# Performance work log

Hardware: AMD Instinct MI355X
Metric: run time of the kernel (lower is better)

The kernel has to match this reference:

```python
import jax, jax.numpy as jnp
import numpy as np

N, E, F_IN, H, C = 100000, 1600000, 128, 128, 40
BN_EPS = 1e-5


def setup_inputs() -> dict:
    key = jax.random.key(0)
    ks = jax.random.split(key, 8)
    x = jax.random.normal(ks[0], (N, F_IN), dtype=jnp.float32)
    edge_index = jax.random.randint(ks[1], (2, E), 0, N, dtype=jnp.int32)
    W1 = jax.random.normal(ks[2], (F_IN, H), dtype=jnp.float32) / np.sqrt(F_IN).astype(np.float32)
    b1 = jnp.zeros((H,), jnp.float32)
    gamma = jnp.ones((H,), jnp.float32)
    beta = jnp.zeros((H,), jnp.float32)
    W2 = jax.random.normal(ks[3], (H, C), dtype=jnp.float32) / np.sqrt(H).astype(np.float32)
    b2 = jnp.zeros((C,), jnp.float32)
    return {"x": x, "edge_index": edge_index, "W1": W1, "b1": b1,
            "gamma": gamma, "beta": beta, "W2": W2, "b2": b2}


def _gcn_conv(h, src, dst, norm, W, b, n):
    # H' = D^-1/2 (A+I) D^-1/2 H W + b   (self-loops already in src/dst/norm)
    h = h @ W                                   # [N, out] small GEMM
    msg = h[src] * norm[:, None]                # [E+N, out] gather
    return jax.ops.segment_sum(msg, dst, num_segments=n) + b


def reference(x, edge_index, W1, b1, gamma, beta, W2, b2):
    n = x.shape[0]
    loop = jnp.arange(n, dtype=edge_index.dtype)
    src = jnp.concatenate([edge_index[0], loop])
    dst = jnp.concatenate([edge_index[1], loop])
    # symmetric normalization of A_tilde = A + I
    deg = jax.ops.segment_sum(jnp.ones_like(dst, jnp.float32), dst, num_segments=n)
    dis = jnp.where(deg > 0, jax.lax.rsqrt(jnp.maximum(deg, 1.0)), 0.0)
    norm = dis[src] * dis[dst]                  # [E+N]

    h = _gcn_conv(x, src, dst, norm, W1, b1, n)
    h = jax.nn.relu(h)
    # BatchNorm1d over nodes (batch statistics; eval, dropout disabled)
    mean = jnp.mean(h, axis=0)
    var = jnp.var(h, axis=0)
    h = (h - mean) * jax.lax.rsqrt(var + BN_EPS) * gamma + beta

    h = _gcn_conv(h, src, dst, norm, W2, b2, n)
    return jax.nn.log_softmax(h, axis=1)
```

## Files before the change

### kernel.cpp

```cpp
#include <hip/hip_runtime.h>
#include <math.h>

#define N_NODES 100000
#define N_EDGES 1600000
#define F_IN 128
#define H_DIM 128
#define C_OUT 40
#define BN_EPS 1e-5f

#define ELL_W 64
#define CNT_STRIDE 16

#define BKT_W 512
#define NBKT ((N_NODES + BKT_W - 1) / BKT_W)
#define BKT_CAP 12288
#define P_EDGES 2048
#define P_NB ((N_EDGES + P_EDGES - 1) / P_EDGES)
#define FP_WCV_NB 64
#define FP_XQ_NB 6250

#define G1_ROWS 128
#define G1_LD 136
#define G1_NB ((N_NODES + G1_ROWS - 1) / G1_ROWS)
#define PS_LD 800
#define G2_ROWS 128
#define G2_NB ((N_NODES + G2_ROWS - 1) / G2_ROWS)
#define H2_B 64

typedef unsigned short u16;
typedef unsigned int u32;
typedef signed char s8;
typedef __attribute__((ext_vector_type(8))) __bf16 bf16x8;
typedef __attribute__((ext_vector_type(4))) float f32x4;

__device__ __forceinline__ u16 f2bf(float f) {
    u32 u = __float_as_uint(f);
    u += 0x7FFFu + ((u >> 16) & 1u);
    return (u16)(u >> 16);
}
__device__ __forceinline__ void qfma4(float* a, u32 d, float w) {
    a[0] = fmaf((float)((int)(d << 24) >> 24), w, a[0]);
    a[1] = fmaf((float)((int)(d << 16) >> 24), w, a[1]);
    a[2] = fmaf((float)((int)(d <<  8) >> 24), w, a[2]);
    a[3] = fmaf((float)((int)d >> 24),         w, a[3]);
}
__device__ __forceinline__ u32 pack4(int q0, int q1, int q2, int q3) {
    return (u32)(q0 & 255) | ((u32)(q1 & 255) << 8) |
           ((u32)(q2 & 255) << 16) | ((u32)(q3 & 255) << 24);
}

__global__ __launch_bounds__(256) void fused_prep(const float* __restrict__ x,
                                                  const float* __restrict__ W1,
                                                  const int* __restrict__ src,
                                                  const int* __restrict__ dst,
                                                  int* __restrict__ bcur,
                                                  int2* __restrict__ region,
                                                  s8* __restrict__ xq,
                                                  float* __restrict__ qs1,
                                                  u16* __restrict__ W1t) {
    __shared__ int lcnt[NBKT];
    __shared__ int gofs[NBKT];
    int b = blockIdx.x, t = threadIdx.x;
    if (b < P_NB) {
        for (int i = t; i < NBKT; i += 256) lcnt[i] = 0;
        __syncthreads();
        int base = b * P_EDGES;
        int d[8], bk[8];
        #pragma unroll
        for (int i = 0; i < 8; ++i) {
            int idx = base + i * 256 + t;
            if (idx < N_EDGES) {
                d[i] = dst[idx];
                bk[i] = d[i] >> 9;
                atomicAdd(&lcnt[bk[i]], 1);
            } else d[i] = -1;
        }
        __syncthreads();
        for (int i = t; i < NBKT; i += 256) {
            int c = lcnt[i];
            gofs[i] = c ? atomicAdd(&bcur[i * CNT_STRIDE], c) : 0;
            lcnt[i] = 0;
        }
        __syncthreads();
        #pragma unroll
        for (int i = 0; i < 8; ++i) {
            int idx = base + i * 256 + t;
            if (idx < N_EDGES) {
                int rank = atomicAdd(&lcnt[bk[i]], 1);
                int pos = gofs[bk[i]] + rank;
                if (pos < BKT_CAP)
                    region[(size_t)bk[i] * BKT_CAP + pos] = make_int2(src[idx], d[i]);
            }
        }
    } else if (b < P_NB + FP_WCV_NB) {
        int i = (b - P_NB) * 256 + t;
        int k = i >> 7, n = i & 127;
        W1t[n * H_DIM + k] = f2bf(W1[k * H_DIM + n]);
    } else {
        int row = (b - P_NB - FP_WCV_NB) * 16 + (t >> 4);
        int lane = t & 15;
        const float4* xr = (const float4*)(x + (size_t)row * F_IN + lane * 8);
        float4 a = xr[0], c = xr[1];
        float m = fmaxf(fmaxf(fmaxf(fabsf(a.x), fabsf(a.y)), fmaxf(fabsf(a.z), fabsf(a.w))),
                        fmaxf(fmaxf(fabsf(c.x), fabsf(c.y)), fmaxf(fabsf(c.z), fabsf(c.w))));
        #pragma unroll
        for (int off = 1; off < 16; off <<= 1) m = fmaxf(m, __shfl_xor(m, off, 16));
        m = fmaxf(m, 1e-20f);
        float inv = 127.f / m;
        u32 p0 = pack4((int)rintf(a.x * inv), (int)rintf(a.y * inv),
                       (int)rintf(a.z * inv), (int)rintf(a.w * inv));
        u32 p1 = pack4((int)rintf(c.x * inv), (int)rintf(c.y * inv),
                       (int)rintf(c.z * inv), (int)rintf(c.w * inv));
        uint2 p; p.x = p0; p.y = p1;
        *(uint2*)(xq + (size_t)row * F_IN + lane * 8) = p;
        if (lane == 0) qs1[row] = m / 127.f;
    }
}

__global__ __launch_bounds__(256) void ell_build(const int* __restrict__ bcur,
                                                 const int2* __restrict__ region,
                                                 int* __restrict__ ell,
                                                 int* __restrict__ cnt,
                                                 float* __restrict__ dinv,
                                                 float* __restrict__ qs1) {
    __shared__ int lcnt[BKT_W];
    int b = blockIdx.x, t = threadIdx.x;
    int nbase = b * BKT_W;
    for (int i = t; i < BKT_W; i += 256) {
        lcnt[i] = 1;
        int node = nbase + i;
        if (node < N_NODES) ell[(size_t)node * ELL_W] = node;
    }
    __syncthreads();
    int ne = bcur[b * CNT_STRIDE];
    if (ne > BKT_CAP) ne = BKT_CAP;
    const int2* reg = region + (size_t)b * BKT_CAP;
    for (int i = t; i < ne; i += 256) {
        int2 p = reg[i];
        int rank = atomicAdd(&lcnt[p.y - nbase], 1);
        if (rank < ELL_W) ell[(size_t)p.y * ELL_W + rank] = p.x;
    }
    __syncthreads();
    for (int i = t; i < BKT_W; i += 256) {
        int node = nbase + i;
        if (node < N_NODES) {
            int c = lcnt[i];
            cnt[node] = (c > ELL_W) ? ELL_W : c;
            float dv = rsqrtf((float)c);
            dinv[node] = dv;
            qs1[node] *= dv;
        }
    }
}

__global__ __launch_bounds__(256) void gather_x(const int* __restrict__ cnt,
                                                const int* __restrict__ ell,
                                                const float* __restrict__ dinv,
                                                const float* __restrict__ qs1,
                                                const s8* __restrict__ xq,
                                                u16* __restrict__ aggb) {
    int node = blockIdx.x * 16 + (threadIdx.x >> 4);
    int q = threadIdx.x & 15;
    int len = cnt[node];
    const int* rowp = ell + (size_t)node * ELL_W;
    float acc[8] = {};
    int e = 0;
    for (; e + 3 < len; e += 4) {
        int s0 = rowp[e], s1 = rowp[e + 1], s2 = rowp[e + 2], s3 = rowp[e + 3];
        float w0 = qs1[s0], w1 = qs1[s1], w2 = qs1[s2], w3 = qs1[s3];
        uint2 v0 = *(const uint2*)(xq + (size_t)s0 * F_IN + q * 8);
        uint2 v1 = *(const uint2*)(xq + (size_t)s1 * F_IN + q * 8);
        uint2 v2 = *(const uint2*)(xq + (size_t)s2 * F_IN + q * 8);
        uint2 v3 = *(const uint2*)(xq + (size_t)s3 * F_IN + q * 8);
        qfma4(acc, v0.x, w0); qfma4(acc + 4, v0.y, w0);
        qfma4(acc, v1.x, w1); qfma4(acc + 4, v1.y, w1);
        qfma4(acc, v2.x, w2); qfma4(acc + 4, v2.y, w2);
        qfma4(acc, v3.x, w3); qfma4(acc + 4, v3.y, w3);
    }
    for (; e < len; ++e) {
        int s = rowp[e];
        float wv = qs1[s];
        uint2 v = *(const uint2*)(xq + (size_t)s * F_IN + q * 8);
        qfma4(acc, v.x, wv); qfma4(acc + 4, v.y, wv);
    }
    float dd = dinv[node];
    int4 o;
    o.x = (int)((u32)f2bf(acc[0] * dd) | ((u32)f2bf(acc[1] * dd) << 16));
    o.y = (int)((u32)f2bf(acc[2] * dd) | ((u32)f2bf(acc[3] * dd) << 16));
    o.z = (int)((u32)f2bf(acc[4] * dd) | ((u32)f2bf(acc[5] * dd) << 16));
    o.w = (int)((u32)f2bf(acc[6] * dd) | ((u32)f2bf(acc[7] * dd) << 16));
    *(int4*)(aggb + (size_t)node * H_DIM + q * 8) = o;
}

__global__ __launch_bounds__(256) void gemm1_mfma(const u16* __restrict__ aggb,
                                                  const u16* __restrict__ W1t,
                                                  const float* __restrict__ b1,
                                                  u16* __restrict__ hb,
                                                  float* __restrict__ pstats) {
    __shared__ u16 As[G1_ROWS * G1_LD];
    int tid = threadIdx.x;
    int base = blockIdx.x * G1_ROWS;

    {
        int row = tid >> 1, half = tid & 1;
        int gr = base + row; if (gr >= N_NODES) gr = N_NODES - 1;
        const int4* gsrc = (const int4*)(aggb + (size_t)gr * H_DIM + half * 64);
        int4* ldst = (int4*)(As + row * G1_LD + half * 64);
        #pragma unroll
        for (int i = 0; i < 8; ++i) ldst[i] = gsrc[i];
    }
    __syncthreads();

    int lane = tid & 63, w = tid >> 6;
    int r = lane & 15, g = lane >> 4;

    bf16x8 wf[2][4];
    #pragma unroll
    for (int t = 0; t < 2; ++t)
        #pragma unroll
        for (int ks = 0; ks < 4; ++ks)
            wf[t][ks] = *(const bf16x8*)(W1t + (w * 32 + t * 16 + r) * H_DIM + ks * 32 + g * 8);

    float bch[2][4];
    #pragma unroll
    for (int t = 0; t < 2; ++t)
        #pragma unroll
        for (int i = 0; i < 4; ++i)
            bch[t][i] = b1[w * 32 + t * 16 + 4 * g + i];

    float cs[8] = {}, cq[8] = {};

    for (int rt = 0; rt < 8; ++rt) {
        f32x4 acc0 = {0.f, 0.f, 0.f, 0.f}, acc1 = {0.f, 0.f, 0.f, 0.f};
        #pragma unroll
        for (int ks = 0; ks < 4; ++ks) {
            bf16x8 nf = *(const bf16x8*)(As + (rt * 16 + r) * G1_LD + ks * 32 + g * 8);
            acc0 = __builtin_amdgcn_mfma_f32_16x16x32_bf16(wf[0][ks], nf, acc0, 0, 0, 0);
            acc1 = __builtin_amdgcn_mfma_f32_16x16x32_bf16(wf[1][ks], nf, acc1, 0, 0, 0);
        }
        int node = base + rt * 16 + r;
        if (node < N_NODES) {
            float o0[4], o1[4];
            #pragma unroll
            for (int i = 0; i < 4; ++i) {
                o0[i] = fmaxf(acc0[i] + bch[0][i], 0.f);
                o1[i] = fmaxf(acc1[i] + bch[1][i], 0.f);
                cs[i]     += o0[i]; cq[i]     += o0[i] * o0[i];
                cs[4 + i] += o1[i]; cq[4 + i] += o1[i] * o1[i];
            }
            uint2 p0, p1;
            p0.x = (u32)f2bf(o0[0]) | ((u32)f2bf(o0[1]) << 16);
            p0.y = (u32)f2bf(o0[2]) | ((u32)f2bf(o0[3]) << 16);
            p1.x = (u32)f2bf(o1[0]) | ((u32)f2bf(o1[1]) << 16);
            p1.y = (u32)f2bf(o1[2]) | ((u32)f2bf(o1[3]) << 16);
            u16* hp = hb + (size_t)node * H_DIM + w * 32 + 4 * g;
            *(uint2*)hp = p0;
            *(uint2*)(hp + 16) = p1;
        }
    }

    #pragma unroll
    for (int j = 0; j < 8; ++j) {
        #pragma unroll
        for (int m = 1; m < 16; m <<= 1) {
            cs[j] += __shfl_xor(cs[j], m, 16);
            cq[j] += __shfl_xor(cq[j], m, 16);
        }
    }
    if (r == 0) {
        #pragma unroll
        for (int j = 0; j < 8; ++j) {
            int c = w * 32 + (j >> 2) * 16 + 4 * g + (j & 3);
            pstats[c * PS_LD + blockIdx.x] = cs[j];
            pstats[(128 + c) * PS_LD + blockIdx.x] = cq[j];
        }
    }
}

__global__ __launch_bounds__(256) void stats_final(const float* __restrict__ pstats,
                                                   const float* __restrict__ gamma,
                                                   const float* __restrict__ beta,
                                                   float* __restrict__ scale,
                                                   float* __restrict__ shift) {
    __shared__ float ls[256], lq[256];
    int c = blockIdx.x, t = threadIdx.x;
    float s = 0.f, q = 0.f;
    for (int b = t; b < G1_NB; b += 256) {
        s += pstats[c * PS_LD + b];
        q += pstats[(128 + c) * PS_LD + b];
    }
    ls[t] = s; lq[t] = q;
    __syncthreads();
    for (int off = 128; off; off >>= 1) {
        if (t < off) { ls[t] += ls[t + off]; lq[t] += lq[t + off]; }
        __syncthreads();
    }
    if (t == 0) {
        const float invn = 1.0f / (float)N_NODES;
        float mean = ls[0] * invn;
        float var = lq[0] * invn - mean * mean;
        float sc = gamma[c] * rsqrtf(var + BN_EPS);
        scale[c] = sc;
        shift[c] = beta[c] - mean * sc;
    }
}

__global__ __launch_bounds__(128) void w2fold(const float* __restrict__ W2,
                                              const float* __restrict__ scale,
                                              const float* __restrict__ shift,
                                              u16* __restrict__ W2t,
                                              float* __restrict__ K) {
    __shared__ float red[128];
    int c = blockIdx.x, k = threadIdx.x;
    float wv = (c < C_OUT) ? W2[k * C_OUT + c] : 0.f;
    W2t[c * H_DIM + k] = (c < C_OUT) ? f2bf(scale[k] * wv) : (u16)0;
    red[k] = shift[k] * wv;
    __syncthreads();
    for (int off = 64; off; off >>= 1) {
        if (k < off) red[k] += red[k + off];
        __syncthreads();
    }
    if (k == 0) K[c] = red[0];
}

__global__ __launch_bounds__(256) void gemm2_mfma(const u16* __restrict__ hb,
                                                  const u16* __restrict__ W2t,
                                                  const float* __restrict__ K,
                                                  const float* __restrict__ dinv,
                                                  s8* __restrict__ h2q,
                                                  float* __restrict__ srow2) {
    __shared__ u16 As[G2_ROWS * G1_LD];
    int tid = threadIdx.x;
    int base = blockIdx.x * G2_ROWS;

    {
        int row = tid >> 1, half = tid & 1;
        int gr = base + row; if (gr >= N_NODES) gr = N_NODES - 1;
        const int4* gsrc = (const int4*)(hb + (size_t)gr * H_DIM + half * 64);
        int4* ldst = (int4*)(As + row * G1_LD + half * 64);
        #pragma unroll
        for (int i = 0; i < 8; ++i) ldst[i] = gsrc[i];
    }
    __syncthreads();

    int lane = tid & 63, w = tid >> 6;
    int r = lane & 15, g = lane >> 4;

    bf16x8 wf[3][4];
    #pragma unroll
    for (int t = 0; t < 3; ++t)
        #pragma unroll
        for (int ks = 0; ks < 4; ++ks)
            wf[t][ks] = *(const bf16x8*)(W2t + (t * 16 + r) * H_DIM + ks * 32 + g * 8);

    float kv[3][4];
    #pragma unroll
    for (int t = 0; t < 3; ++t)
        #pragma unroll
        for (int i = 0; i < 4; ++i)
            kv[t][i] = K[t * 16 + 4 * g + i];

    f32x4 acc[2][3];
    #pragma unroll
    for (int i2 = 0; i2 < 2; ++i2)
        #pragma unroll
        for (int t = 0; t < 3; ++t)
            acc[i2][t] = (f32x4){0.f, 0.f, 0.f, 0.f};

    #pragma unroll
    for (int i2 = 0; i2 < 2; ++i2) {
        int rt = 2 * w + i2;
        #pragma unroll
        for (int ks = 0; ks < 4; ++ks) {
            bf16x8 nf = *(const bf16x8*)(As + (rt * 16 + r) * G1_LD + ks * 32 + g * 8);
            acc[i2][0] = __builtin_amdgcn_mfma_f32_16x16x32_bf16(wf[0][ks], nf, acc[i2][0], 0, 0, 0);
            acc[i2][1] = __builtin_amdgcn_mfma_f32_16x16x32_bf16(wf[1][ks], nf, acc[i2][1], 0, 0, 0);
            acc[i2][2] = __builtin_amdgcn_mfma_f32_16x16x32_bf16(wf[2][ks], nf, acc[i2][2], 0, 0, 0);
        }
    }

    #pragma unroll
    for (int i2 = 0; i2 < 2; ++i2) {
        int node = base + (2 * w + i2) * 16 + r;
        float dd = (node < N_NODES) ? dinv[node] : 0.f;
        float v[3][4];
        float m = 0.f;
        #pragma unroll
        for (int t = 0; t < 3; ++t)
            #pragma unroll
            for (int i = 0; i < 4; ++i) {
                v[t][i] = (acc[i2][t][i] + kv[t][i]) * dd;
                if (t < 2 || g < 2) m = fmaxf(m, fabsf(v[t][i]));
            }
        m = fmaxf(m, __shfl_xor(m, 16));
        m = fmaxf(m, __shfl_xor(m, 32));
        m = fmaxf(m, 1e-20f);
        float inv = 127.f / m;
        if (node < N_NODES) {
            s8* hp = h2q + (size_t)node * H2_B;
            #pragma unroll
            for (int t = 0; t < 2; ++t) {
                u32 p = pack4((int)rintf(v[t][0] * inv), (int)rintf(v[t][1] * inv),
                              (int)rintf(v[t][2] * inv), (int)rintf(v[t][3] * inv));
                *(u32*)(hp + t * 16 + 4 * g) = p;
            }
            u32 p2 = (g < 2) ? pack4((int)rintf(v[2][0] * inv), (int)rintf(v[2][1] * inv),
                                     (int)rintf(v[2][2] * inv), (int)rintf(v[2][3] * inv))
                             : 0u;
            *(u32*)(hp + 32 + 4 * g) = p2;
            *(u32*)(hp + 48 + 4 * g) = 0u;
            if (g == 0) srow2[node] = m / 127.f;
        }
    }
}

__global__ __launch_bounds__(256) void gather2_fused(const int* __restrict__ cnt,
                                                     const int* __restrict__ ell,
                                                     const float* __restrict__ dinv,
                                                     const float* __restrict__ srow2,
                                                     const s8* __restrict__ h2q,
                                                     const float* __restrict__ b2,
                                                     float* __restrict__ out) {
    int node = blockIdx.x * 16 + (threadIdx.x >> 4);
    int q = threadIdx.x & 15;
    int len = cnt[node];
    const int* rowp = ell + (size_t)node * ELL_W;
    float acc[4] = {};
    int e = 0;
    for (; e + 3 < len; e += 4) {
        int s0 = rowp[e], s1 = rowp[e + 1], s2 = rowp[e + 2], s3 = rowp[e + 3];
        float w0 = srow2[s0], w1 = srow2[s1], w2 = srow2[s2], w3 = srow2[s3];
        u32 d0 = *(const u32*)(h2q + (size_t)s0 * H2_B + q * 4);
        u32 d1 = *(const u32*)(h2q + (size_t)s1 * H2_B + q * 4);
        u32 d2 = *(const u32*)(h2q + (size_t)s2 * H2_B + q * 4);
        u32 d3 = *(const u32*)(h2q + (size_t)s3 * H2_B + q * 4);
        qfma4(acc, d0, w0); qfma4(acc, d1, w1);
        qfma4(acc, d2, w2); qfma4(acc, d3, w3);
    }
    for (; e < len; ++e) {
        int s = rowp[e];
        float wv = srow2[s];
        u32 d = *(const u32*)(h2q + (size_t)s * H2_B + q * 4);
        qfma4(acc, d, wv);
    }
    float dd = dinv[node];
    float4 r;
    float m = -INFINITY;
    if (q < 10) {
        float4 bv = *(const float4*)(b2 + q * 4);
        r.x = fmaf(acc[0], dd, bv.x); r.y = fmaf(acc[1], dd, bv.y);
        r.z = fmaf(acc[2], dd, bv.z); r.w = fmaf(acc[3], dd, bv.w);
        m = fmaxf(fmaxf(r.x, r.y), fmaxf(r.z, r.w));
    }
    #pragma unroll
    for (int off = 1; off < 16; off <<= 1) m = fmaxf(m, __shfl_xor(m, off, 16));
    float ex = 0.f;
    if (q < 10)
        ex = expf(r.x - m) + expf(r.y - m) + expf(r.z - m) + expf(r.w - m);
    #pragma unroll
    for (int off = 1; off < 16; off <<= 1) ex += __shfl_xor(ex, off, 16);
    float lse = logf(ex) + m;
    if (q < 10) {
        float4 o = {r.x - lse, r.y - lse, r.z - lse, r.w - lse};
        *(float4*)(out + (size_t)node * C_OUT + q * 4) = o;
    }
}

extern "C" void kernel_launch(void* const* d_in, const int* in_sizes, int n_in,
                              void* d_out, int out_size, void* d_ws, size_t ws_size,
                              hipStream_t stream) {
    const float* x     = (const float*)d_in[0];
    const int*   eidx  = (const int*)d_in[1];
    const float* W1    = (const float*)d_in[2];
    const float* b1    = (const float*)d_in[3];
    const float* gamma = (const float*)d_in[4];
    const float* beta  = (const float*)d_in[5];
    const float* W2    = (const float*)d_in[6];
    const float* b2    = (const float*)d_in[7];
    float* out = (float*)d_out;

    const int* src = eidx;
    const int* dst = eidx + N_EDGES;

    float* ws = (float*)d_ws;
    float* dinv    = ws;
    int*   cnt     = (int*)(ws + 100000);
    int*   bcur    = (int*)(ws + 200000);
    int*   ell     = (int*)(ws + 203200);
    s8*    xq      = (s8*)(ws + 6603200);
    float* qs1     = ws + 9803200;
    float* srow2   = ws + 9903200;
    u16*   aggb    = (u16*)(ws + 10003200);
    int2*  region  = (int2*)(ws + 10003200);
    u16*   hb      = (u16*)(ws + 16403200);
    u16*   W1t     = (u16*)(ws + 22803200);
    s8*    h2q     = (s8*)(ws + 22811392);
    float* pstats  = ws + 24411392;
    float* scale   = ws + 24616192;
    float* shift   = ws + 24616320;
    float* K       = ws + 24616448;
    u16*   W2t     = (u16*)(ws + 24616512);

    size_t needed = (size_t)(24616512 + 3072 + 256) * 4;
    if (ws_size < needed) return;

    hipMemsetAsync(bcur, 0, NBKT * CNT_STRIDE * 4, stream);
    fused_prep<<<P_NB + FP_WCV_NB + FP_XQ_NB, 256, 0, stream>>>(
        x, W1, src, dst, bcur, region, xq, qs1, W1t);
    ell_build<<<NBKT, 256, 0, stream>>>(bcur, region, ell, cnt, dinv, qs1);

    gather_x<<<N_NODES / 16, 256, 0, stream>>>(cnt, ell, dinv, qs1, xq, aggb);
    gemm1_mfma<<<G1_NB, 256, 0, stream>>>(aggb, W1t, b1, hb, pstats);
    stats_final<<<128, 256, 0, stream>>>(pstats, gamma, beta, scale, shift);
    w2fold<<<48, 128, 0, stream>>>(W2, scale, shift, W2t, K);

    gemm2_mfma<<<G2_NB, 256, 0, stream>>>(hb, W2t, K, dinv, h2q, srow2);
    gather2_fused<<<N_NODES / 16, 256, 0, stream>>>(cnt, ell, dinv, srow2, h2q, b2, out);
}
```

Measured before the change: 174.6 us.

## Stage bucketed edges in LDS and pack src/local-dst into one word

The edge bucketing pass now sorts each block's edges by bucket in shared memory, using a prefix scan over bucket counts, before writing them out. The writes to the bucket region become contiguous runs instead of scattered 8-byte stores. Each edge is packed into a single 32-bit word (9-bit local destination, 17-bit source), which halves region traffic in both the prep and ELL build kernels. Edges per block are doubled to amortize the scan, at the cost of more shared memory, a serial 8-step scan with barriers, and fewer prep blocks.

```diff
diff --git a/kernel.cpp b/kernel.cpp
--- a/kernel.cpp
+++ b/kernel.cpp
@@ -14,7 +14,7 @@
 #define BKT_W 512
 #define NBKT ((N_NODES + BKT_W - 1) / BKT_W)
 #define BKT_CAP 12288
-#define P_EDGES 2048
+#define P_EDGES 4096
 #define P_NB ((N_EDGES + P_EDGES - 1) / P_EDGES)
 #define FP_WCV_NB 64
 #define FP_XQ_NB 6250
@@ -54,43 +54,65 @@
                                                   const int* __restrict__ src,
                                                   const int* __restrict__ dst,
                                                   int* __restrict__ bcur,
-                                                  int2* __restrict__ region,
+                                                  u32* __restrict__ region,
                                                   s8* __restrict__ xq,
                                                   float* __restrict__ qs1,
                                                   u16* __restrict__ W1t) {
+    __shared__ u32 stage[P_EDGES];
+    __shared__ u16 bkarr[P_EDGES];
     __shared__ int lcnt[NBKT];
-    __shared__ int gofs[NBKT];
+    __shared__ int loffs[NBKT];
+    __shared__ int baseaddr[NBKT];
+    __shared__ int tmp[256];
+    __shared__ int tot_sh;
     int b = blockIdx.x, t = threadIdx.x;
     if (b < P_NB) {
         for (int i = t; i < NBKT; i += 256) lcnt[i] = 0;
         __syncthreads();
         int base = b * P_EDGES;
-        int d[8], bk[8];
-        #pragma unroll
-        for (int i = 0; i < 8; ++i) {
+        #pragma unroll
+        for (int i = 0; i < 16; ++i) {
+            int idx = base + i * 256 + t;
+            if (idx < N_EDGES) atomicAdd(&lcnt[dst[idx] >> 9], 1);
+        }
+        __syncthreads();
+        int v = (t < NBKT) ? lcnt[t] : 0;
+        tmp[t] = v;
+        __syncthreads();
+        for (int off = 1; off < 256; off <<= 1) {
+            int u = (t >= off) ? tmp[t - off] : 0;
+            __syncthreads();
+            tmp[t] += u;
+            __syncthreads();
+        }
+        if (t < NBKT) {
+            int lo = tmp[t] - v;
+            loffs[t] = lo;
+            int g = v ? atomicAdd(&bcur[t * CNT_STRIDE], v) : 0;
+            baseaddr[t] = t * BKT_CAP + g - lo;
+            lcnt[t] = 0;
+        }
+        if (t == 255) tot_sh = tmp[255];
+        __syncthreads();
+        #pragma unroll
+        for (int i = 0; i < 16; ++i) {
             int idx = base + i * 256 + t;
             if (idx < N_EDGES) {
-                d[i] = dst[idx];
-                bk[i] = d[i] >> 9;
-                atomicAdd(&lcnt[bk[i]], 1);
-            } else d[i] = -1;
-        }
-        __syncthreads();
-        for (int i = t; i < NBKT; i += 256) {
-            int c = lcnt[i];
-            gofs[i] = c ? atomicAdd(&bcur[i * CNT_STRIDE], c) : 0;
-            lcnt[i] = 0;
-        }
-        __syncthreads();
-        #pragma unroll
-        for (int i = 0; i < 8; ++i) {
-            int idx = base + i * 256 + t;
-            if (idx < N_EDGES) {
-                int rank = atomicAdd(&lcnt[bk[i]], 1);
-                int pos = gofs[bk[i]] + rank;
-                if (pos < BKT_CAP)
-                    region[(size_t)bk[i] * BKT_CAP + pos] = make_int2(src[idx], d[i]);
+                int d = dst[idx];
+                int bk = d >> 9;
+                int rank = atomicAdd(&lcnt[bk], 1);
+                int slot = loffs[bk] + rank;
+                stage[slot] = ((u32)(d & 511) << 17) | (u32)src[idx];
+                bkarr[slot] = (u16)bk;
             }
+        }
+        __syncthreads();
+        int tot = tot_sh;
+        for (int j = t; j < tot; j += 256) {
+            int bk = bkarr[j];
+            int destp = baseaddr[bk] + j;
+            if (destp - bk * BKT_CAP < BKT_CAP)
+                region[destp] = stage[j];
         }
     } else if (b < P_NB + FP_WCV_NB) {
         int i = (b - P_NB) * 256 + t;
@@ -118,7 +140,7 @@
 }
 
 __global__ __launch_bounds__(256) void ell_build(const int* __restrict__ bcur,
-                                                 const int2* __restrict__ region,
+                                                 const u32* __restrict__ region,
                                                  int* __restrict__ ell,
                                                  int* __restrict__ cnt,
                                                  float* __restrict__ dinv,
@@ -134,11 +156,13 @@
     __syncthreads();
     int ne = bcur[b * CNT_STRIDE];
     if (ne > BKT_CAP) ne = BKT_CAP;
-    const int2* reg = region + (size_t)b * BKT_CAP;
+    const u32* reg = region + (size_t)b * BKT_CAP;
     for (int i = t; i < ne; i += 256) {
-        int2 p = reg[i];
-        int rank = atomicAdd(&lcnt[p.y - nbase], 1);
-        if (rank < ELL_W) ell[(size_t)p.y * ELL_W + rank] = p.x;
+        u32 p = reg[i];
+        int ldst = (int)(p >> 17);
+        int srcv = (int)(p & 0x1FFFFu);
+        int rank = atomicAdd(&lcnt[ldst], 1);
+        if (rank < ELL_W) ell[(size_t)(nbase + ldst) * ELL_W + rank] = srcv;
     }
     __syncthreads();
     for (int i = t; i < BKT_W; i += 256) {
@@ -491,7 +515,7 @@
     float* qs1     = ws + 9803200;
     float* srow2   = ws + 9903200;
     u16*   aggb    = (u16*)(ws + 10003200);
-    int2*  region  = (int2*)(ws + 10003200);
+    u32*   region  = (u32*)(ws + 10003200);
     u16*   hb      = (u16*)(ws + 16403200);
     u16*   W1t     = (u16*)(ws + 22803200);
     s8*    h2q     = (s8*)(ws + 22811392);
```

New measurement: 169.6 us. 2.9% less time.
